# Performance work log

Hardware: AMD Instinct MI355X
Metric: run time of the kernel (lower is better)

## Reference

```python
import jax, jax.numpy as jnp
import numpy as np

VOCAB, EMB, HIDDEN, OUT = 50000, 300, 512, 2
SEQ, BATCH = 512, 1024


def setup_inputs() -> dict:
    key = jax.random.key(0)
    k_text, k_len, k_emb, k_w1, k_b1, k_w2, k_b2 = jax.random.split(key, 7)
    text = jax.random.randint(k_text, (SEQ, BATCH), 1, VOCAB, dtype=jnp.int64 if jax.config.jax_enable_x64 else jnp.int32)
    lengths = jax.random.randint(k_len, (BATCH,), 1, SEQ + 1, dtype=text.dtype)
    emb_table = jax.random.normal(k_emb, (VOCAB, EMB), dtype=jnp.float32) * 0.1
    emb_table = emb_table.at[0].set(0.0)  # padding_idx=0 row zeroed like nn.Embedding
    W1 = jax.random.normal(k_w1, (EMB, HIDDEN), dtype=jnp.float32) * (1.0 / np.sqrt(EMB))
    b1 = jax.random.normal(k_b1, (HIDDEN,), dtype=jnp.float32) * 0.01
    W2 = jax.random.normal(k_w2, (HIDDEN, OUT), dtype=jnp.float32) * (1.0 / np.sqrt(HIDDEN))
    b2 = jax.random.normal(k_b2, (OUT,), dtype=jnp.float32) * 0.01
    return {"text": text, "lengths": lengths, "emb_table": emb_table,
            "W1": W1, "b1": b1, "W2": W2, "b2": b2}


def reference(text, lengths, emb_table, W1, b1, W2, b2):
    # text: [S, B] int; embedding lookup -> [S, B, E]
    embedded = emb_table[text]
    # masked mean over the first `lengths[b]` tokens (vectorized segment mean)
    seq = embedded.shape[0]
    mask = (jnp.arange(seq)[:, None] < lengths[None, :]).astype(embedded.dtype)  # [S, B]
    pooled = jnp.einsum('sbe,sb->be', embedded, mask) / lengths[:, None].astype(embedded.dtype)  # [B, E]
    # fc1 -> (dropout p=0, identity) -> relu -> fc2
    h = jax.nn.relu(pooled @ W1 + b1)
    return h @ W2 + b2
```

## Files before the change

### kernel.cpp

```cpp
#include <hip/hip_runtime.h>

typedef float f32x4 __attribute__((ext_vector_type(4)));

constexpr int EMB    = 300;
constexpr int EMB4   = 75;
constexpr int HIDDEN = 512;
constexpr int SEQ    = 512;
constexpr int BATCH  = 1024;
constexpr int VOCAB  = 50000;
constexpr int NBUK   = 32;
constexpr int BDIV   = 1563;
constexpr int PB     = 4;
constexpr int GMLP   = 8;
constexpr int NCONV  = 1792;
constexpr int ELEM4  = VOCAB * EMB / 4;

__device__ __forceinline__ unsigned short f2bf(float x) {
    unsigned u = __float_as_uint(x);
    u += 0x7fffu + ((u >> 16) & 1u);
    return (unsigned short)(u >> 16);
}

__global__ __launch_bounds__(256) void prep_kernel(
    const int* __restrict__ text,
    const int* __restrict__ lengths,
    const float* __restrict__ emb,
    int* __restrict__ btok,
    int* __restrict__ boff,
    unsigned short* __restrict__ ebf,
    int doConv)
{
    __shared__ int4 tstage[SEQ];
    __shared__ int  hist[4][8][NBUK + 2];

    const int tid = threadIdx.x;

    if (blockIdx.x >= 256) {
        if (!doConv) return;
        const float4* src = (const float4*)emb;
        ushort4*      dst = (ushort4*)ebf;
        const int gtid = (blockIdx.x - 256) * 256 + tid;
        for (int i = gtid; i < ELEM4; i += NCONV * 256) {
            const float4 v = src[i];
            ushort4 o;
            o.x = f2bf(v.x); o.y = f2bf(v.y);
            o.z = f2bf(v.z); o.w = f2bf(v.w);
            dst[i] = o;
        }
        return;
    }

    const int wave = tid >> 6;
    const int lane = tid & 63;
    const int b0   = blockIdx.x * 4;
    const int b    = b0 + wave;
    const int len  = lengths[b];
    const unsigned long long lt = (1ull << lane) - 1ull;

    for (int s = tid; s < SEQ; s += 256)
        tstage[s] = *(const int4*)&text[(size_t)s * BATCH + b0];
    for (int i = tid; i < 4 * 8 * (NBUK + 2); i += 256)
        ((int*)hist)[i] = 0;
    __syncthreads();

    int tokv[8], kv[8], rkv[8];
#pragma unroll
    for (int c = 0; c < 8; ++c) {
        const int s      = c * 64 + lane;
        const bool valid = s < len;
        const int tok = valid ? ((const int*)&tstage[s])[wave] : 0;
        const int k   = valid ? tok / BDIV : NBUK;
        unsigned long long mm = ~0ull;
#pragma unroll
        for (int bit = 0; bit < 6; ++bit) {
            const unsigned long long bl = __ballot((k >> bit) & 1);
            mm &= ((k >> bit) & 1) ? bl : ~bl;
        }
        const int rk = __popcll(mm & lt);
        tokv[c] = tok; kv[c] = k; rkv[c] = rk;
        if (valid && rk == 0) hist[wave][c][k] = __popcll(mm);
    }
    __syncthreads();

    int tot = 0;
    if (lane < NBUK) {
#pragma unroll
        for (int c = 0; c < 8; ++c) {
            const int t = hist[wave][c][lane];
            hist[wave][c][lane] = tot;
            tot += t;
        }
    }
    int incl = tot;
#pragma unroll
    for (int off = 1; off < 32; off <<= 1) {
        const int v = __shfl_up(incl, off);
        if (lane >= off && lane < NBUK) incl += v;
    }
    const int excl = incl - tot;
    if (lane < NBUK)      boff[b * (NBUK + 1) + lane] = excl;
    if (lane == NBUK - 1) boff[b * (NBUK + 1) + NBUK] = incl;
    __syncthreads();

#pragma unroll
    for (int c = 0; c < 8; ++c) {
        const int s  = c * 64 + lane;
        const int k  = kv[c];
        const int bb = __shfl(excl, k);
        const int pos = bb + hist[wave][c][k] + rkv[c];
        if (s < len) btok[(size_t)b * SEQ + pos] = tokv[c];
    }
}

__device__ __forceinline__ f32x4 bf4up(uint2 u) {
    f32x4 r;
    r.x = __uint_as_float(u.x << 16);
    r.y = __uint_as_float(u.x & 0xffff0000u);
    r.z = __uint_as_float(u.y << 16);
    r.w = __uint_as_float(u.y & 0xffff0000u);
    return r;
}

template<bool BF>
__global__ __launch_bounds__(320) void pool_kernel(
    const int* __restrict__ btok,
    const int* __restrict__ boff,
    const float* __restrict__ emb,
    const unsigned short* __restrict__ ebf,
    float* __restrict__ partial,
    int NX)
{
    const int x  = blockIdx.x % NX;
    const int b0 = (blockIdx.x / NX) * PB;
    const int NJ = NBUK / NX;

    __shared__ int toks[PB][SEQ];
    __shared__ int seg[PB][2];

    if (threadIdx.x < PB) {
        const int b  = b0 + threadIdx.x;
        const int lo = boff[b * (NBUK + 1) + x * NJ];
        const int hi = boff[b * (NBUK + 1) + x * NJ + NJ];
        seg[threadIdx.x][0] = lo;
        seg[threadIdx.x][1] = hi - lo;
    }
    __syncthreads();

    for (int g = 0; g < PB; ++g) {
        const int lo = seg[g][0], n = seg[g][1];
        for (int t = threadIdx.x; t < n; t += 320)
            toks[g][t] = btok[(size_t)(b0 + g) * SEQ + lo + t];
    }
    __syncthreads();

    const int g = threadIdx.x / 80;
    const int c = threadIdx.x % 80;
    if (c < EMB4) {
        const int n = seg[g][1];
        f32x4 A = {0.f, 0.f, 0.f, 0.f};
        f32x4 B = A;
        int i = 0;
        if constexpr (BF) {
            const uint2* e2 = (const uint2*)ebf;
            for (; i + 4 <= n; i += 4) {
                const int4 t4 = *(const int4*)&toks[g][i];
                const uint2 u0 = e2[(size_t)t4.x * EMB4 + c];
                const uint2 u1 = e2[(size_t)t4.y * EMB4 + c];
                const uint2 u2 = e2[(size_t)t4.z * EMB4 + c];
                const uint2 u3 = e2[(size_t)t4.w * EMB4 + c];
                A += bf4up(u0) + bf4up(u1);
                B += bf4up(u2) + bf4up(u3);
            }
            for (; i < n; ++i)
                A += bf4up(e2[(size_t)toks[g][i] * EMB4 + c]);
        } else {
            const f32x4* e4 = (const f32x4*)emb;
            for (; i + 4 <= n; i += 4) {
                const int4 t4 = *(const int4*)&toks[g][i];
                const f32x4 v0 = e4[(size_t)t4.x * EMB4 + c];
                const f32x4 v1 = e4[(size_t)t4.y * EMB4 + c];
                const f32x4 v2 = e4[(size_t)t4.z * EMB4 + c];
                const f32x4 v3 = e4[(size_t)t4.w * EMB4 + c];
                A += v0 + v1;
                B += v2 + v3;
            }
            for (; i < n; ++i)
                A += e4[(size_t)toks[g][i] * EMB4 + c];
        }
        A += B;
        ((f32x4*)(partial + ((size_t)x * BATCH + b0 + g) * EMB))[c] = A;
    }
}

template<int NX>
__global__ __launch_bounds__(512) void mlp_kernel(
    const float* __restrict__ partial,
    const int* __restrict__ lengths,
    const float* __restrict__ W1,
    const float* __restrict__ b1,
    const float* __restrict__ W2,
    const float* __restrict__ b2,
    float* __restrict__ out)
{
    __shared__ f32x4 pQ[GMLP / 4][EMB];
    __shared__ float hsh[GMLP][HIDDEN];

    const int b0  = blockIdx.x * GMLP;
    const int tid = threadIdx.x;

    float* pQf = (float*)pQ;
    for (int i = tid; i < EMB * GMLP; i += 512) {
        const int g = i / EMB;
        const int e = i - g * EMB;
        float s = 0.f;
#pragma unroll
        for (int xx = 0; xx < NX; ++xx)
            s += partial[((size_t)xx * BATCH + b0 + g) * EMB + e];
        pQf[((g >> 2) * EMB + e) * 4 + (g & 3)] = s / (float)lengths[b0 + g];
    }
    __syncthreads();

    const int j = tid;
    const float bias = b1[j];
    f32x4 acc0 = {bias, bias, bias, bias};
    f32x4 acc1 = acc0;

#pragma unroll 10
    for (int e = 0; e < EMB; ++e) {
        const float w = W1[(size_t)e * HIDDEN + j];
        acc0 += pQ[0][e] * w;
        acc1 += pQ[1][e] * w;
    }
    hsh[0][j] = fmaxf(acc0.x, 0.f);
    hsh[1][j] = fmaxf(acc0.y, 0.f);
    hsh[2][j] = fmaxf(acc0.z, 0.f);
    hsh[3][j] = fmaxf(acc0.w, 0.f);
    hsh[4][j] = fmaxf(acc1.x, 0.f);
    hsh[5][j] = fmaxf(acc1.y, 0.f);
    hsh[6][j] = fmaxf(acc1.z, 0.f);
    hsh[7][j] = fmaxf(acc1.w, 0.f);
    __syncthreads();

    const int w    = tid >> 6;
    const int lane = tid & 63;
    const f32x4* W2v = (const f32x4*)W2;
    float s0 = 0.f, s1 = 0.f;
#pragma unroll
    for (int q = 0; q < 2; ++q) {
        const int cc = lane + q * 64;
        const f32x4 hv = *(const f32x4*)&hsh[w][4 * cc];
        const f32x4 wA = W2v[2 * cc + 0];
        const f32x4 wB = W2v[2 * cc + 1];
        s0 += hv.x * wA.x + hv.y * wA.z + hv.z * wB.x + hv.w * wB.z;
        s1 += hv.x * wA.y + hv.y * wA.w + hv.z * wB.y + hv.w * wB.w;
    }
#pragma unroll
    for (int off = 32; off > 0; off >>= 1) {
        s0 += __shfl_down(s0, off);
        s1 += __shfl_down(s1, off);
    }
    if (lane == 0) {
        out[(b0 + w) * 2 + 0] = s0 + b2[0];
        out[(b0 + w) * 2 + 1] = s1 + b2[1];
    }
}

extern "C" void kernel_launch(void* const* d_in, const int* in_sizes, int n_in,
                              void* d_out, int out_size, void* d_ws, size_t ws_size,
                              hipStream_t stream) {
    const int*   text    = (const int*)d_in[0];
    const int*   lengths = (const int*)d_in[1];
    const float* emb     = (const float*)d_in[2];
    const float* W1      = (const float*)d_in[3];
    const float* b1      = (const float*)d_in[4];
    const float* W2      = (const float*)d_in[5];
    const float* b2      = (const float*)d_in[6];
    float*       out     = (float*)d_out;

    char* ws = (char*)d_ws;
    const size_t btokBytes = (size_t)BATCH * SEQ * sizeof(int);
    const size_t boffBytes = (size_t)BATCH * (NBUK + 1) * sizeof(int);
    const size_t ebfBytes  = (size_t)VOCAB * EMB * sizeof(unsigned short);
    const size_t poolBytes = (size_t)BATCH * EMB * sizeof(float);

    int* btok = (int*)ws;
    int* boff = (int*)(ws + btokBytes);
    size_t off = btokBytes + boffBytes;
    off = (off + 63) & ~(size_t)63;
    unsigned short* ebf = (unsigned short*)(ws + off);

    const size_t fixedBF = off + ebfBytes;
    bool useBF = false;
    int NX = 1;
    float* partial;
    if (ws_size >= fixedBF + 2 * poolBytes) {
        useBF = true;
        partial = (float*)(ws + fixedBF);
        if      (ws_size >= fixedBF + 8 * poolBytes) NX = 8;
        else if (ws_size >= fixedBF + 4 * poolBytes) NX = 4;
        else                                         NX = 2;
    } else {
        partial = (float*)(ws + off);
        if      (ws_size >= off + 8 * poolBytes) NX = 8;
        else if (ws_size >= off + 4 * poolBytes) NX = 4;
        else if (ws_size >= off + 2 * poolBytes) NX = 2;
    }

    prep_kernel<<<useBF ? 256 + NCONV : 256, 256, 0, stream>>>(
        text, lengths, emb, btok, boff, ebf, useBF ? 1 : 0);

    if (useBF)
        pool_kernel<true><<<NX * (BATCH / PB), 320, 0, stream>>>(btok, boff, emb, ebf, partial, NX);
    else
        pool_kernel<false><<<NX * (BATCH / PB), 320, 0, stream>>>(btok, boff, emb, ebf, partial, NX);

    switch (NX) {
        case 8:  mlp_kernel<8><<<BATCH / GMLP, 512, 0, stream>>>(partial, lengths, W1, b1, W2, b2, out); break;
        case 4:  mlp_kernel<4><<<BATCH / GMLP, 512, 0, stream>>>(partial, lengths, W1, b1, W2, b2, out); break;
        case 2:  mlp_kernel<2><<<BATCH / GMLP, 512, 0, stream>>>(partial, lengths, W1, b1, W2, b2, out); break;
        default: mlp_kernel<1><<<BATCH / GMLP, 512, 0, stream>>>(partial, lengths, W1, b1, W2, b2, out); break;
    }
}
```

Before: 61.48 us.

## Bind pool work to XCC via per-partition atomic ticket queues

The pooling kernel becomes persistent. Each block reads its XCC ID and claims batch groups from a per-vocab-partition atomic ticket counter, starting with the partition that matches its XCC. This keeps each XCC's gathers within one eighth of the bf16 embedding table so its L2 stays warm. Partial sums are written with nontemporal stores, and a simple fallback pool kernel replaces the older multi-NX paths. The risks are atomic and barrier overhead per work item, and reliance on the XCC count matching NX.

```diff
diff --git a/kernel.cpp b/kernel.cpp
--- a/kernel.cpp
+++ b/kernel.cpp
@@ -11,6 +11,8 @@
 constexpr int NBUK   = 32;
 constexpr int BDIV   = 1563;
 constexpr int PB     = 4;
+constexpr int NX     = 8;
+constexpr int NGRP   = BATCH / PB;
 constexpr int GMLP   = 8;
 constexpr int NCONV  = 1792;
 constexpr int ELEM4  = VOCAB * EMB / 4;
@@ -19,6 +21,15 @@
     unsigned u = __float_as_uint(x);
     u += 0x7fffu + ((u >> 16) & 1u);
     return (unsigned short)(u >> 16);
+}
+
+__device__ __forceinline__ f32x4 bf4up(uint2 u) {
+    f32x4 r;
+    r.x = __uint_as_float(u.x << 16);
+    r.y = __uint_as_float(u.x & 0xffff0000u);
+    r.z = __uint_as_float(u.y << 16);
+    r.w = __uint_as_float(u.y & 0xffff0000u);
+    return r;
 }
 
 __global__ __launch_bounds__(256) void prep_kernel(
@@ -28,6 +39,7 @@
     int* __restrict__ btok,
     int* __restrict__ boff,
     unsigned short* __restrict__ ebf,
+    int* __restrict__ tickets,
     int doConv)
 {
     __shared__ int4 tstage[SEQ];
@@ -37,6 +49,7 @@
 
     if (blockIdx.x >= 256) {
         if (!doConv) return;
+        if (blockIdx.x == 256 && tid < NX) tickets[tid] = 0;
         const float4* src = (const float4*)emb;
         ushort4*      dst = (ushort4*)ebf;
         const int gtid = (blockIdx.x - 256) * 256 + tid;
@@ -112,87 +125,77 @@
     }
 }
 
-__device__ __forceinline__ f32x4 bf4up(uint2 u) {
-    f32x4 r;
-    r.x = __uint_as_float(u.x << 16);
-    r.y = __uint_as_float(u.x & 0xffff0000u);
-    r.z = __uint_as_float(u.y << 16);
-    r.w = __uint_as_float(u.y & 0xffff0000u);
-    return r;
-}
-
-template<bool BF>
 __global__ __launch_bounds__(320) void pool_kernel(
     const int* __restrict__ btok,
     const int* __restrict__ boff,
-    const float* __restrict__ emb,
     const unsigned short* __restrict__ ebf,
     float* __restrict__ partial,
-    int NX)
+    int* __restrict__ tickets)
 {
-    const int x  = blockIdx.x % NX;
-    const int b0 = (blockIdx.x / NX) * PB;
-    const int NJ = NBUK / NX;
-
     __shared__ int toks[PB][SEQ];
     __shared__ int seg[PB][2];
-
-    if (threadIdx.x < PB) {
-        const int b  = b0 + threadIdx.x;
-        const int lo = boff[b * (NBUK + 1) + x * NJ];
-        const int hi = boff[b * (NBUK + 1) + x * NJ + NJ];
-        seg[threadIdx.x][0] = lo;
-        seg[threadIdx.x][1] = hi - lo;
-    }
-    __syncthreads();
-
-    for (int g = 0; g < PB; ++g) {
-        const int lo = seg[g][0], n = seg[g][1];
-        for (int t = threadIdx.x; t < n; t += 320)
-            toks[g][t] = btok[(size_t)(b0 + g) * SEQ + lo + t];
-    }
-    __syncthreads();
-
-    const int g = threadIdx.x / 80;
-    const int c = threadIdx.x % 80;
-    if (c < EMB4) {
-        const int n = seg[g][1];
-        f32x4 A = {0.f, 0.f, 0.f, 0.f};
-        f32x4 B = A;
-        int i = 0;
-        if constexpr (BF) {
-            const uint2* e2 = (const uint2*)ebf;
-            for (; i + 4 <= n; i += 4) {
-                const int4 t4 = *(const int4*)&toks[g][i];
-                const uint2 u0 = e2[(size_t)t4.x * EMB4 + c];
-                const uint2 u1 = e2[(size_t)t4.y * EMB4 + c];
-                const uint2 u2 = e2[(size_t)t4.z * EMB4 + c];
-                const uint2 u3 = e2[(size_t)t4.w * EMB4 + c];
-                A += bf4up(u0) + bf4up(u1);
-                B += bf4up(u2) + bf4up(u3);
+    __shared__ int claimsh;
+
+    int xcc;
+    asm volatile("s_getreg_b32 %0, hwreg(HW_REG_XCC_ID)" : "=s"(xcc));
+    xcc &= (NX - 1);
+
+    const int tid = threadIdx.x;
+    const int grp = tid / 80;
+    const int c   = tid % 80;
+    const int NJ  = NBUK / NX;
+
+    for (int t = 0; t < NX; ++t) {
+        const int x = (xcc + t) & (NX - 1);
+        while (true) {
+            __syncthreads();
+            if (tid == 0) claimsh = atomicAdd(&tickets[x], 1);
+            __syncthreads();
+            const int g = claimsh;
+            if (g >= NGRP) break;
+            const int b0 = g * PB;
+
+            if (tid < PB) {
+                const int b  = b0 + tid;
+                const int lo = boff[b * (NBUK + 1) + x * NJ];
+                const int hi = boff[b * (NBUK + 1) + x * NJ + NJ];
+                seg[tid][0] = lo;
+                seg[tid][1] = hi - lo;
             }
-            for (; i < n; ++i)
-                A += bf4up(e2[(size_t)toks[g][i] * EMB4 + c]);
-        } else {
-            const f32x4* e4 = (const f32x4*)emb;
-            for (; i + 4 <= n; i += 4) {
-                const int4 t4 = *(const int4*)&toks[g][i];
-                const f32x4 v0 = e4[(size_t)t4.x * EMB4 + c];
-                const f32x4 v1 = e4[(size_t)t4.y * EMB4 + c];
-                const f32x4 v2 = e4[(size_t)t4.z * EMB4 + c];
-                const f32x4 v3 = e4[(size_t)t4.w * EMB4 + c];
-                A += v0 + v1;
-                B += v2 + v3;
+            __syncthreads();
+            for (int g2 = 0; g2 < PB; ++g2) {
+                const int lo = seg[g2][0], n = seg[g2][1];
+                for (int tt = tid; tt < n; tt += 320)
+                    toks[g2][tt] = btok[(size_t)(b0 + g2) * SEQ + lo + tt];
             }
-            for (; i < n; ++i)
-                A += e4[(size_t)toks[g][i] * EMB4 + c];
+            __syncthreads();
+
+            if (c < EMB4) {
+                const int n = seg[grp][1];
+                const uint2* e2 = (const uint2*)ebf;
+                f32x4 A = {0.f, 0.f, 0.f, 0.f};
+                f32x4 B = A;
+                int i = 0;
+                for (; i + 4 <= n; i += 4) {
+                    const int4 t4 = *(const int4*)&toks[grp][i];
+                    const uint2 u0 = e2[(size_t)t4.x * EMB4 + c];
+                    const uint2 u1 = e2[(size_t)t4.y * EMB4 + c];
+                    const uint2 u2 = e2[(size_t)t4.z * EMB4 + c];
+                    const uint2 u3 = e2[(size_t)t4.w * EMB4 + c];
+                    A += bf4up(u0) + bf4up(u1);
+                    B += bf4up(u2) + bf4up(u3);
+                }
+                for (; i < n; ++i)
+                    A += bf4up(e2[(size_t)toks[grp][i] * EMB4 + c]);
+                A += B;
+                f32x4* dst = (f32x4*)(partial + ((size_t)x * BATCH + b0 + grp) * EMB) + c;
+                __builtin_nontemporal_store(A, dst);
+            }
         }
-        A += B;
-        ((f32x4*)(partial + ((size_t)x * BATCH + b0 + g) * EMB))[c] = A;
-    }
-}
-
-template<int NX>
+    }
+}
+
+template<int NXT>
 __global__ __launch_bounds__(512) void mlp_kernel(
     const float* __restrict__ partial,
     const int* __restrict__ lengths,
@@ -214,7 +217,7 @@
         const int e = i - g * EMB;
         float s = 0.f;
 #pragma unroll
-        for (int xx = 0; xx < NX; ++xx)
+        for (int xx = 0; xx < NXT; ++xx)
             s += partial[((size_t)xx * BATCH + b0 + g) * EMB + e];
         pQf[((g >> 2) * EMB + e) * 4 + (g & 3)] = s / (float)lengths[b0 + g];
     }
@@ -262,6 +265,25 @@
     if (lane == 0) {
         out[(b0 + w) * 2 + 0] = s0 + b2[0];
         out[(b0 + w) * 2 + 1] = s1 + b2[1];
+    }
+}
+
+__global__ __launch_bounds__(320) void naive_pool(
+    const int* __restrict__ text, const int* __restrict__ lengths,
+    const float* __restrict__ emb, float* __restrict__ pooled)
+{
+    __shared__ int toks[SEQ];
+    const int b = blockIdx.x;
+    const int len = lengths[b];
+    for (int s = threadIdx.x; s < len; s += 320)
+        toks[s] = text[(size_t)s * BATCH + b];
+    __syncthreads();
+    const int e = threadIdx.x;
+    if (e < EMB) {
+        float a = 0.f;
+        for (int s = 0; s < len; ++s)
+            a += emb[(size_t)toks[s] * EMB + e];
+        pooled[(size_t)b * EMB + e] = a;
     }
 }
 
@@ -280,6 +302,7 @@
     char* ws = (char*)d_ws;
     const size_t btokBytes = (size_t)BATCH * SEQ * sizeof(int);
     const size_t boffBytes = (size_t)BATCH * (NBUK + 1) * sizeof(int);
+    const size_t tickBytes = 64;
     const size_t ebfBytes  = (size_t)VOCAB * EMB * sizeof(unsigned short);
     const size_t poolBytes = (size_t)BATCH * EMB * sizeof(float);
 
@@ -287,37 +310,23 @@
     int* boff = (int*)(ws + btokBytes);
     size_t off = btokBytes + boffBytes;
     off = (off + 63) & ~(size_t)63;
+    int* tickets = (int*)(ws + off);
+    off += tickBytes;
     unsigned short* ebf = (unsigned short*)(ws + off);
-
-    const size_t fixedBF = off + ebfBytes;
-    bool useBF = false;
-    int NX = 1;
-    float* partial;
-    if (ws_size >= fixedBF + 2 * poolBytes) {
-        useBF = true;
-        partial = (float*)(ws + fixedBF);
-        if      (ws_size >= fixedBF + 8 * poolBytes) NX = 8;
-        else if (ws_size >= fixedBF + 4 * poolBytes) NX = 4;
-        else                                         NX = 2;
+    float* partial = (float*)(ws + off + ebfBytes);
+
+    const size_t need = off + ebfBytes + (size_t)NX * poolBytes;
+
+    if (ws_size >= need) {
+        prep_kernel<<<256 + NCONV, 256, 0, stream>>>(
+            text, lengths, emb, btok, boff, ebf, tickets, 1);
+        pool_kernel<<<1536, 320, 0, stream>>>(btok, boff, ebf, partial, tickets);
+        mlp_kernel<8><<<BATCH / GMLP, 512, 0, stream>>>(
+            partial, lengths, W1, b1, W2, b2, out);
     } else {
-        partial = (float*)(ws + off);
-        if      (ws_size >= off + 8 * poolBytes) NX = 8;
-        else if (ws_size >= off + 4 * poolBytes) NX = 4;
-        else if (ws_size >= off + 2 * poolBytes) NX = 2;
-    }
-
-    prep_kernel<<<useBF ? 256 + NCONV : 256, 256, 0, stream>>>(
-        text, lengths, emb, btok, boff, ebf, useBF ? 1 : 0);
-
-    if (useBF)
-        pool_kernel<true><<<NX * (BATCH / PB), 320, 0, stream>>>(btok, boff, emb, ebf, partial, NX);
-    else
-        pool_kernel<false><<<NX * (BATCH / PB), 320, 0, stream>>>(btok, boff, emb, ebf, partial, NX);
-
-    switch (NX) {
-        case 8:  mlp_kernel<8><<<BATCH / GMLP, 512, 0, stream>>>(partial, lengths, W1, b1, W2, b2, out); break;
-        case 4:  mlp_kernel<4><<<BATCH / GMLP, 512, 0, stream>>>(partial, lengths, W1, b1, W2, b2, out); break;
-        case 2:  mlp_kernel<2><<<BATCH / GMLP, 512, 0, stream>>>(partial, lengths, W1, b1, W2, b2, out); break;
-        default: mlp_kernel<1><<<BATCH / GMLP, 512, 0, stream>>>(partial, lengths, W1, b1, W2, b2, out); break;
-    }
-}
+        float* pooled = (float*)ws;
+        naive_pool<<<BATCH, 320, 0, stream>>>(text, lengths, emb, pooled);
+        mlp_kernel<1><<<BATCH / GMLP, 512, 0, stream>>>(
+            pooled, lengths, W1, b1, W2, b2, out);
+    }
+}
```

Result: slower. 212.9 us (+246.4%).
